# Performance work log

Measured on AMD Instinct MI355X. Metric: run time of the kernel, lower is better.

Reference implementation:

```python
import jax, jax.numpy as jnp
import numpy as np

TEMPERATURE = 3.0
SINKHORN_ITERS = 20
NOISE_SCALE = 1.0
EPS = 1e-20


def setup_inputs() -> dict:
    key = jax.random.key(0)
    k1, k2, k3 = jax.random.split(key, 3)
    x = jax.random.normal(k1, (524288, 128), dtype=jnp.float32)
    logits = jax.random.normal(k2, (128, 128), dtype=jnp.float32)
    u = jax.random.uniform(k3, (128, 128), dtype=jnp.float32)
    return {"x": x, "logits": logits, "u": u}


def reference(x, logits, u):
    # Gumbel noise from uniform sample (matches sample_gumbel)
    gumbel = -jnp.log(-jnp.log(u + EPS) + EPS) * NOISE_SCALE
    log_alpha = (logits + gumbel) / TEMPERATURE
    log_alpha = jnp.clip(log_alpha, -10.0, 10.0)
    A = jnp.exp(log_alpha)
    # Sinkhorn: alternate row / column normalization (fixed 20 iters)
    for _ in range(SINKHORN_ITERS):
        A = A / jnp.sum(A, axis=1, keepdims=True)
        A = A / jnp.sum(A, axis=0, keepdims=True)
    P = jnp.nan_to_num(A, nan=0.0, posinf=1.0, neginf=0.0)
    # [batch, num_inputs] @ [num_inputs, num_leaves]
    return x @ P.T
```

## Files before the change

kernel.cpp:

```cpp
#include <hip/hip_runtime.h>
#include <hip/hip_bf16.h>

typedef _Float16 half8 __attribute__((ext_vector_type(8)));
typedef float floatx4 __attribute__((ext_vector_type(4)));

__global__ __launch_bounds__(1024, 1) void sinkhorn128(
    const float* __restrict__ logits, const float* __restrict__ u,
    _Float16* __restrict__ Pout) {
    __shared__ float sA[128 * 129];
    __shared__ alignas(16) float sR[128];
    __shared__ alignas(16) float sC[128];
    const int t = threadIdx.x;

    #pragma unroll
    for (int k = 0; k < 16; ++k) {
        int e = t + (k << 10);
        float lg = logits[e];
        float uu = u[e];
        float g  = -logf(-logf(uu + 1e-20f) + 1e-20f);
        float la = (lg + g) * (1.0f / 3.0f);
        la = fminf(10.0f, fmaxf(-10.0f, la));
        sA[(e >> 7) * 129 + (e & 127)] = expf(la);
    }
    if (t < 128) sC[t] = 1.0f;
    __syncthreads();

    const bool isRow = (t < 512);
    const int i = (t & 511) >> 2;
    const int q = t & 3;

    float a[32];
    if (isRow) {
        #pragma unroll
        for (int j = 0; j < 32; ++j) a[j] = sA[i * 129 + q * 32 + j];
    } else {
        #pragma unroll
        for (int j = 0; j < 32; ++j) a[j] = sA[(q * 32 + j) * 129 + i];
    }

    float ri = 1.0f;
    for (int it = 0; it < 20; ++it) {
        if (isRow) {
            float s0 = 0.f, s1 = 0.f, s2 = 0.f, s3 = 0.f;
            #pragma unroll
            for (int j = 0; j < 32; j += 4) {
                float4 c4 = *reinterpret_cast<const float4*>(&sC[q * 32 + j]);
                s0 = fmaf(a[j + 0], c4.x, s0);
                s1 = fmaf(a[j + 1], c4.y, s1);
                s2 = fmaf(a[j + 2], c4.z, s2);
                s3 = fmaf(a[j + 3], c4.w, s3);
            }
            float p = (s0 + s1) + (s2 + s3);
            p += __shfl_xor(p, 1);
            p += __shfl_xor(p, 2);
            ri = 1.0f / p;
            if (q == 0) sR[i] = ri;
        }
        __syncthreads();
        if (!isRow) {
            float s0 = 0.f, s1 = 0.f, s2 = 0.f, s3 = 0.f;
            #pragma unroll
            for (int j = 0; j < 32; j += 4) {
                float4 r4 = *reinterpret_cast<const float4*>(&sR[q * 32 + j]);
                s0 = fmaf(a[j + 0], r4.x, s0);
                s1 = fmaf(a[j + 1], r4.y, s1);
                s2 = fmaf(a[j + 2], r4.z, s2);
                s3 = fmaf(a[j + 3], r4.w, s3);
            }
            float p = (s0 + s1) + (s2 + s3);
            p += __shfl_xor(p, 1);
            p += __shfl_xor(p, 2);
            if (q == 0) sC[i] = 1.0f / p;
        }
        __syncthreads();
    }

    if (isRow) {
        #pragma unroll
        for (int j = 0; j < 32; j += 2) {
            union { _Float16 h[2]; unsigned int w; } pk;
            pk.h[0] = (_Float16)(ri * a[j + 0] * sC[q * 32 + j + 0]);
            pk.h[1] = (_Float16)(ri * a[j + 1] * sC[q * 32 + j + 1]);
            reinterpret_cast<unsigned int*>(Pout)[(i * 128 + q * 32 + j) >> 1] = pk.w;
        }
    }
}

__global__ __launch_bounds__(256, 1) void streamMatmul(
    const float* __restrict__ x, const _Float16* __restrict__ P,
    float* __restrict__ out) {
    const int lane = threadIdx.x & 63;
    const int wv   = threadIdx.x >> 6;
    const int gw   = blockIdx.x * 4 + wv;
    const int r    = lane & 15;
    const int q    = lane >> 4;

    half8 Bf[4][8];
    #pragma unroll
    for (int ks = 0; ks < 4; ++ks)
        #pragma unroll
        for (int nt = 0; nt < 8; ++nt)
            Bf[ks][nt] = *reinterpret_cast<const half8*>(
                P + (nt * 16 + r) * 128 + ks * 32 + q * 8);

    const long baseRow = (long)gw * 256;
    const float* xp0 = x + (baseRow + r) * 128 + q * 8;

    floatx4 xa[4][2];
    #pragma unroll
    for (int ks = 0; ks < 4; ++ks) {
        xa[ks][0] = *reinterpret_cast<const floatx4*>(xp0 + ks * 32);
        xa[ks][1] = *reinterpret_cast<const floatx4*>(xp0 + ks * 32 + 4);
    }

    for (int t = 0; t < 16; ++t) {
        half8 ah[4], al[4];
        #pragma unroll
        for (int ks = 0; ks < 4; ++ks)
            #pragma unroll
            for (int jj = 0; jj < 8; ++jj) {
                float f = (jj < 4) ? xa[ks][0][jj] : xa[ks][1][jj - 4];
                _Float16 h = (_Float16)f;
                ah[ks][jj] = h;
                al[ks][jj] = (_Float16)(f - (float)h);
            }

        if (t < 15) {
            const float* xp = xp0 + (t + 1) * 16 * 128;
            #pragma unroll
            for (int ks = 0; ks < 4; ++ks) {
                xa[ks][0] = *reinterpret_cast<const floatx4*>(xp + ks * 32);
                xa[ks][1] = *reinterpret_cast<const floatx4*>(xp + ks * 32 + 4);
            }
        }

        floatx4 acc[8];
        #pragma unroll
        for (int nt = 0; nt < 8; ++nt) acc[nt] = (floatx4){0.f, 0.f, 0.f, 0.f};

        #pragma unroll
        for (int ks = 0; ks < 4; ++ks)
            #pragma unroll
            for (int nt = 0; nt < 8; ++nt) {
                acc[nt] = __builtin_amdgcn_mfma_f32_16x16x32_f16(
                    ah[ks], Bf[ks][nt], acc[nt], 0, 0, 0);
                acc[nt] = __builtin_amdgcn_mfma_f32_16x16x32_f16(
                    al[ks], Bf[ks][nt], acc[nt], 0, 0, 0);
            }

        const long m0 = baseRow + t * 16;
        float* op = out + (m0 + q * 4) * 128 + r;
        #pragma unroll
        for (int nt = 0; nt < 8; ++nt)
            #pragma unroll
            for (int rr = 0; rr < 4; ++rr)
                __builtin_nontemporal_store(acc[nt][rr], op + rr * 128 + nt * 16);
    }
}

extern "C" void kernel_launch(void* const* d_in, const int* in_sizes, int n_in,
                              void* d_out, int out_size, void* d_ws, size_t ws_size,
                              hipStream_t stream) {
    (void)in_sizes; (void)n_in; (void)out_size; (void)ws_size;
    const float* x      = (const float*)d_in[0];
    const float* logits = (const float*)d_in[1];
    const float* u      = (const float*)d_in[2];
    float* out          = (float*)d_out;
    _Float16* P         = (_Float16*)d_ws;

    sinkhorn128<<<1, 1024, 0, stream>>>(logits, u, P);
    streamMatmul<<<512, 256, 0, stream>>>(x, P, out);
}
```

Baseline: 494.0 us.

## Stage P in swizzled LDS, raise occupancy, interleave row tiles across grid

The matmul kernel no longer holds all of P's fragments in registers. Each block copies P into an XOR-swizzled shared-memory tile and reads B fragments from LDS for each k-step, which frees registers so launch bounds can allow 3 blocks per CU. The grid doubles to 1024 blocks with 8 tiles per wave, and tiles are interleaved with a global stride so concurrent waves touch adjacent memory. The cost is extra LDS reads per MFMA group, plus a per-block P load and barrier.

Measured after the change: 497.4 us. About the same (+0.7%).

```diff
diff --git a/kernel.cpp b/kernel.cpp
--- a/kernel.cpp
+++ b/kernel.cpp
@@ -86,25 +86,35 @@
     }
 }
 
-__global__ __launch_bounds__(256, 1) void streamMatmul(
+__global__ __launch_bounds__(256, 3) void streamMatmul(
     const float* __restrict__ x, const _Float16* __restrict__ P,
     float* __restrict__ out) {
-    const int lane = threadIdx.x & 63;
-    const int wv   = threadIdx.x >> 6;
-    const int gw   = blockIdx.x * 4 + wv;
+    __shared__ _Float16 sB[128 * 128];
+    const int tid  = threadIdx.x;
+    const int lane = tid & 63;
     const int r    = lane & 15;
     const int q    = lane >> 4;
+    const int s    = r & 7;
 
-    half8 Bf[4][8];
     #pragma unroll
-    for (int ks = 0; ks < 4; ++ks)
-        #pragma unroll
-        for (int nt = 0; nt < 8; ++nt)
-            Bf[ks][nt] = *reinterpret_cast<const half8*>(
-                P + (nt * 16 + r) * 128 + ks * 32 + q * 8);
+    for (int c = 0; c < 8; ++c) {
+        int e   = tid + c * 256;
+        int row = e >> 4;
+        int cc  = e & 15;
+        half8 v = *reinterpret_cast<const half8*>(P + e * 8);
+        *reinterpret_cast<half8*>(reinterpret_cast<char*>(sB) +
+                                  row * 256 + ((cc ^ (row & 7)) << 4)) = v;
+    }
+    __syncthreads();
 
-    const long baseRow = (long)gw * 256;
-    const float* xp0 = x + (baseRow + r) * 128 + q * 8;
+    int co[4];
+    #pragma unroll
+    for (int ks = 0; ks < 4; ++ks) co[ks] = ((ks * 4 + q) ^ s) << 4;
+    const int rowb = r * 256;
+    const char* sBb = reinterpret_cast<const char*>(sB);
+
+    const int gw = blockIdx.x * 4 + (tid >> 6);
+    const float* xp0 = x + (long)gw * 16 * 128 + r * 128 + q * 8;
 
     floatx4 xa[4][2];
     #pragma unroll
@@ -113,7 +123,7 @@
         xa[ks][1] = *reinterpret_cast<const floatx4*>(xp0 + ks * 32 + 4);
     }
 
-    for (int t = 0; t < 16; ++t) {
+    for (int t = 0; t < 8; ++t) {
         half8 ah[4], al[4];
         #pragma unroll
         for (int ks = 0; ks < 4; ++ks)
@@ -125,8 +135,8 @@
                 al[ks][jj] = (_Float16)(f - (float)h);
             }
 
-        if (t < 15) {
-            const float* xp = xp0 + (t + 1) * 16 * 128;
+        if (t < 7) {
+            const float* xp = xp0 + (long)(t + 1) * 4096 * 2048;
             #pragma unroll
             for (int ks = 0; ks < 4; ++ks) {
                 xa[ks][0] = *reinterpret_cast<const floatx4*>(xp + ks * 32);
@@ -139,16 +149,22 @@
         for (int nt = 0; nt < 8; ++nt) acc[nt] = (floatx4){0.f, 0.f, 0.f, 0.f};
 
         #pragma unroll
-        for (int ks = 0; ks < 4; ++ks)
+        for (int ks = 0; ks < 4; ++ks) {
+            half8 bf[8];
+            #pragma unroll
+            for (int nt = 0; nt < 8; ++nt)
+                bf[nt] = *reinterpret_cast<const half8*>(
+                    sBb + rowb + co[ks] + nt * 4096);
             #pragma unroll
             for (int nt = 0; nt < 8; ++nt) {
                 acc[nt] = __builtin_amdgcn_mfma_f32_16x16x32_f16(
-                    ah[ks], Bf[ks][nt], acc[nt], 0, 0, 0);
+                    ah[ks], bf[nt], acc[nt], 0, 0, 0);
                 acc[nt] = __builtin_amdgcn_mfma_f32_16x16x32_f16(
-                    al[ks], Bf[ks][nt], acc[nt], 0, 0, 0);
+                    al[ks], bf[nt], acc[nt], 0, 0, 0);
             }
+        }
 
-        const long m0 = baseRow + t * 16;
+        const long m0 = (long)(gw + t * 4096) * 16;
         float* op = out + (m0 + q * 4) * 128 + r;
         #pragma unroll
         for (int nt = 0; nt < 8; ++nt)
@@ -169,5 +185,5 @@
     _Float16* P         = (_Float16*)d_ws;
 
     sinkhorn128<<<1, 1024, 0, stream>>>(logits, u, P);
-    streamMatmul<<<512, 256, 0, stream>>>(x, P, out);
+    streamMatmul<<<1024, 256, 0, stream>>>(x, P, out);
 }
```
